# Kernel optimization log

Hardware: AMD Instinct MI355X
Metric: run time of the kernel (lower is better)

## Reference

```python
import jax, jax.numpy as jnp
import numpy as np

MAX_DISTANCE = 5
DISTANCE_TAU = 2.0
H, W = 4096, 4096


def _shifts_at_distance(distance):
    # All (dx, dy) with |dx| + |dy| == distance (diamond ring)
    return [(dx, dy)
            for dx in range(-distance, distance + 1)
            for dy in range(-distance, distance + 1)
            if abs(dx) + abs(dy) == distance]


def setup_inputs() -> dict:
    key = jax.random.key(0)
    grid_spikes = jax.random.normal(key, (H, W), dtype=jnp.float32)
    # Parameter init: w_d = exp(-d / tau), d = 1..max_distance
    distances = jnp.arange(1, MAX_DISTANCE + 1, dtype=jnp.float32)
    distance_weights = jnp.exp(-distances / DISTANCE_TAU)
    return {"grid_spikes": grid_spikes, "distance_weights": distance_weights}


def reference(grid_spikes, distance_weights):
    # I_internal = sum_{d=1}^{D} w_d * sum_{|dx|+|dy|=d} roll(s, (dx, dy))
    contributions = []
    for distance in range(1, MAX_DISTANCE + 1):
        ring = jnp.zeros_like(grid_spikes)
        for dx, dy in _shifts_at_distance(distance):
            ring = ring + jnp.roll(grid_spikes, shift=(dx, dy), axis=(0, 1))
        contributions.append(ring)
    all_neighbors = jnp.stack(contributions, axis=0)          # [D, H, W]
    total_input = (all_neighbors * distance_weights[:, None, None]).sum(axis=0)
    return total_input
```

## Files before the change

kernel.cpp:

```cpp
#include <hip/hip_runtime.h>
#include <stdint.h>


#define GMASK  4095
#define TR     8
#define NRW    (TR + 10)
#define SW     512
#define LW     (SW + 16)

typedef float f4 __attribute__((ext_vector_type(4), aligned(16)));

#define GLOBAL_AS __attribute__((address_space(1)))
#define LDS_AS    __attribute__((address_space(3)))

__device__ __forceinline__ void stage16(const float* g, float* l) {
    __builtin_amdgcn_global_load_lds((const GLOBAL_AS uint32_t*)g,
                                     (LDS_AS uint32_t*)l, 16, 0, 0);
}

__device__ __forceinline__ float uniform_f(float x) {
    union { float f; int i; } u;
    u.f = x;
    u.i = __builtin_amdgcn_readfirstlane(u.i);
    return u.f;
}

__global__ __launch_bounds__(128)
void diamond_stencil(const float* __restrict__ s, const float* __restrict__ w,
                     float* __restrict__ out)
{
    __shared__ float tile[NRW][LW];

    const int tid  = threadIdx.x;
    const int lane = tid & 63;
    const int wv   = tid >> 6;

    const int bid = blockIdx.x;
    const int xcd = bid & 7;
    const int i   = bid >> 3;
    const int bx  = i & 7;
    const int ys  = i >> 3;

    const int j0 = bx << 9;
    const int t0 = xcd * 512 + ys * TR;

#pragma unroll
    for (int m = 0; m < 9; ++m) {
        const int r = wv + 2 * m;
        const float* srow = s + ((size_t)((t0 - 5 + r) & GMASK) << 12);
        float* lrow = &tile[r][8];
        stage16(srow + j0 + lane * 4,       lrow);
        stage16(srow + j0 + 256 + lane * 4, lrow + 256);
    }

    if (tid < NRW * 4) {
        const int r  = tid >> 2, p = tid & 3;
        const int gc = (p < 2 ? j0 - 8 + p * 4 : j0 + SW + (p - 2) * 4) & GMASK;
        const int lc = (p < 2 ? p * 4 : 8 + SW + (p - 2) * 4);
        const float* srow = s + ((size_t)((t0 - 5 + r) & GMASK) << 12);
        *(f4*)&tile[r][lc] = *(const f4*)(srow + gc);
    }

    __syncthreads();

    float wgt[6];
    wgt[0] = 1.0f;
#pragma unroll
    for (int d = 1; d <= 5; ++d) wgt[d] = uniform_f(w[d - 1]);

    float acc[TR][4];
#pragma unroll
    for (int a = 0; a < TR; ++a)
#pragma unroll
        for (int c = 0; c < 4; ++c) acc[a][c] = 0.0f;

    const int tc = tid * 4;

#pragma unroll
    for (int r = 0; r < NRW; ++r) {
        const f4* lp = (const f4*)&tile[r][tc];
        const f4 A = lp[0], B = lp[1], C = lp[2], D = lp[3], E = lp[4];
        float f[20];
        f[0]=A.x; f[1]=A.y; f[2]=A.z; f[3]=A.w;
        f[4]=B.x; f[5]=B.y; f[6]=B.z; f[7]=B.w;
        f[8]=C.x; f[9]=C.y; f[10]=C.z; f[11]=C.w;
        f[12]=D.x; f[13]=D.y; f[14]=D.z; f[15]=D.w;
        f[16]=E.x; f[17]=E.y; f[18]=E.z; f[19]=E.w;

#pragma unroll
        for (int c = 0; c < 4; ++c) {
            const float ctr = f[8 + c];
            float Hs[6];
            Hs[0] = ctr;
#pragma unroll
            for (int k = 1; k <= 5; ++k)
                Hs[k] = Hs[k - 1] + wgt[k] * (f[8 + c - k] + f[8 + c + k]);

#pragma unroll
            for (int a = 0; a < TR; ++a) {
                const int d = r - 5 - a;
                if (d < -5 || d > 5) continue;
                if (d == 0)
                    acc[a][c] += Hs[5] - ctr;
                else {
                    const int ad = d < 0 ? -d : d;
                    acc[a][c] += wgt[ad] * Hs[5 - ad];
                }
            }
        }
    }

#pragma unroll
    for (int a = 0; a < TR; ++a) {
        float* op = out + ((size_t)(t0 + a) << 12) + j0 + tc;
        f4 r0;
        r0.x = acc[a][0]; r0.y = acc[a][1]; r0.z = acc[a][2]; r0.w = acc[a][3];
        __builtin_nontemporal_store(r0, (f4*)op);
    }
}

extern "C" void kernel_launch(void* const* d_in, const int* in_sizes, int n_in,
                              void* d_out, int out_size, void* d_ws, size_t ws_size,
                              hipStream_t stream)
{
    const float* s = (const float*)d_in[0];
    const float* w = (const float*)d_in[1];
    float* out = (float*)d_out;

    dim3 grid(4096);
    dim3 block(128);
    diamond_stencil<<<grid, block, 0, stream>>>(s, w, out);
}
```

Measured before the change: 121.6 us.

## Stream row bands through an LDS ring buffer with persistent blocks

Each block now walks down a 64-row band in eight 8-row tiles and keeps input rows in a 32-row LDS ring. The next tile's rows are loaded asynchronously while the current tile computes, so the 10-row halo is fetched once per band instead of once per tile. The grid shrinks from 4096 blocks to 512, and the output stores switch from nontemporal to plain stores. In exchange there are fewer blocks to fill the GPU, more serial work per block, and a barrier after every tile.

```diff
diff --git a/kernel.cpp b/kernel.cpp
--- a/kernel.cpp
+++ b/kernel.cpp
@@ -4,7 +4,8 @@
 
 #define GMASK  4095
 #define TR     8
-#define NRW    (TR + 10)
+#define NTILE  8
+#define RING   32
 #define SW     512
 #define LW     (SW + 16)
 
@@ -29,93 +30,103 @@
 void diamond_stencil(const float* __restrict__ s, const float* __restrict__ w,
                      float* __restrict__ out)
 {
-    __shared__ float tile[NRW][LW];
+    __shared__ float ring[RING][LW];
 
     const int tid  = threadIdx.x;
     const int lane = tid & 63;
     const int wv   = tid >> 6;
 
-    const int bid = blockIdx.x;
-    const int xcd = bid & 7;
-    const int i   = bid >> 3;
-    const int bx  = i & 7;
-    const int ys  = i >> 3;
+    const int bid   = blockIdx.x;
+    const int xcd   = bid & 7;
+    const int idx   = bid >> 3;
+    const int strip = idx & 7;
+    const int band  = xcd * 8 + (idx >> 3);
 
-    const int j0 = bx << 9;
-    const int t0 = xcd * 512 + ys * TR;
-
-#pragma unroll
-    for (int m = 0; m < 9; ++m) {
-        const int r = wv + 2 * m;
-        const float* srow = s + ((size_t)((t0 - 5 + r) & GMASK) << 12);
-        float* lrow = &tile[r][8];
-        stage16(srow + j0 + lane * 4,       lrow);
-        stage16(srow + j0 + 256 + lane * 4, lrow + 256);
-    }
-
-    if (tid < NRW * 4) {
-        const int r  = tid >> 2, p = tid & 3;
-        const int gc = (p < 2 ? j0 - 8 + p * 4 : j0 + SW + (p - 2) * 4) & GMASK;
-        const int lc = (p < 2 ? p * 4 : 8 + SW + (p - 2) * 4);
-        const float* srow = s + ((size_t)((t0 - 5 + r) & GMASK) << 12);
-        *(f4*)&tile[r][lc] = *(const f4*)(srow + gc);
-    }
-
-    __syncthreads();
+    const int j0  = strip << 9;
+    const int rb  = band << 6;
+    const int rb5 = rb - 5;
 
     float wgt[6];
     wgt[0] = 1.0f;
 #pragma unroll
     for (int d = 1; d <= 5; ++d) wgt[d] = uniform_f(w[d - 1]);
 
-    float acc[TR][4];
-#pragma unroll
-    for (int a = 0; a < TR; ++a)
-#pragma unroll
-        for (int c = 0; c < 4; ++c) acc[a][c] = 0.0f;
-
     const int tc = tid * 4;
 
+    auto stage_rows = [&](int n0, int cnt) {
+        for (int n = n0 + wv; n < n0 + cnt; n += 2) {
+            const float* srow = s + ((size_t)((rb5 + n) & GMASK) << 12);
+            float* lrow = &ring[n & (RING - 1)][8];
+            stage16(srow + j0 + lane * 4,       lrow);
+            stage16(srow + j0 + 256 + lane * 4, lrow + 256);
+        }
+        if (tid < cnt * 4) {
+            const int rr = tid >> 2, p = tid & 3;
+            const int n  = n0 + rr;
+            const int gc = (p < 2 ? j0 - 8 + p * 4 : j0 + SW + (p - 2) * 4) & GMASK;
+            const int lc = (p < 2 ? p * 4 : 8 + SW + (p - 2) * 4);
+            const float* srow = s + ((size_t)((rb5 + n) & GMASK) << 12);
+            *(f4*)&ring[n & (RING - 1)][lc] = *(const f4*)(srow + gc);
+        }
+    };
+
+    stage_rows(0, 18);
+    __syncthreads();
+
+    for (int t = 0; t < NTILE; ++t) {
+        if (t < NTILE - 1) stage_rows(18 + 8 * t, 8);
+
+        float acc[TR][4];
 #pragma unroll
-    for (int r = 0; r < NRW; ++r) {
-        const f4* lp = (const f4*)&tile[r][tc];
-        const f4 A = lp[0], B = lp[1], C = lp[2], D = lp[3], E = lp[4];
-        float f[20];
-        f[0]=A.x; f[1]=A.y; f[2]=A.z; f[3]=A.w;
-        f[4]=B.x; f[5]=B.y; f[6]=B.z; f[7]=B.w;
-        f[8]=C.x; f[9]=C.y; f[10]=C.z; f[11]=C.w;
-        f[12]=D.x; f[13]=D.y; f[14]=D.z; f[15]=D.w;
-        f[16]=E.x; f[17]=E.y; f[18]=E.z; f[19]=E.w;
+        for (int a = 0; a < TR; ++a)
+#pragma unroll
+            for (int c = 0; c < 4; ++c) acc[a][c] = 0.0f;
+
+        const int n0 = 8 * t;
+#pragma unroll
+        for (int k = 0; k < TR + 10; ++k) {
+            const int slot = (n0 + k) & (RING - 1);
+            const f4* lp = (const f4*)&ring[slot][tc];
+            const f4 A = lp[0], B = lp[1], C = lp[2], D = lp[3], E = lp[4];
+            float f[20];
+            f[0]=A.x;  f[1]=A.y;  f[2]=A.z;  f[3]=A.w;
+            f[4]=B.x;  f[5]=B.y;  f[6]=B.z;  f[7]=B.w;
+            f[8]=C.x;  f[9]=C.y;  f[10]=C.z; f[11]=C.w;
+            f[12]=D.x; f[13]=D.y; f[14]=D.z; f[15]=D.w;
+            f[16]=E.x; f[17]=E.y; f[18]=E.z; f[19]=E.w;
 
 #pragma unroll
-        for (int c = 0; c < 4; ++c) {
-            const float ctr = f[8 + c];
-            float Hs[6];
-            Hs[0] = ctr;
+            for (int c = 0; c < 4; ++c) {
+                const float ctr = f[8 + c];
+                float Hs[6];
+                Hs[0] = ctr;
 #pragma unroll
-            for (int k = 1; k <= 5; ++k)
-                Hs[k] = Hs[k - 1] + wgt[k] * (f[8 + c - k] + f[8 + c + k]);
+                for (int q = 1; q <= 5; ++q)
+                    Hs[q] = Hs[q - 1] + wgt[q] * (f[8 + c - q] + f[8 + c + q]);
 
 #pragma unroll
-            for (int a = 0; a < TR; ++a) {
-                const int d = r - 5 - a;
-                if (d < -5 || d > 5) continue;
-                if (d == 0)
-                    acc[a][c] += Hs[5] - ctr;
-                else {
-                    const int ad = d < 0 ? -d : d;
-                    acc[a][c] += wgt[ad] * Hs[5 - ad];
+                for (int a = 0; a < TR; ++a) {
+                    const int d = k - 5 - a;
+                    if (d < -5 || d > 5) continue;
+                    if (d == 0)
+                        acc[a][c] += Hs[5] - ctr;
+                    else {
+                        const int ad = d < 0 ? -d : d;
+                        acc[a][c] += wgt[ad] * Hs[5 - ad];
+                    }
                 }
             }
         }
-    }
 
 #pragma unroll
-    for (int a = 0; a < TR; ++a) {
-        float* op = out + ((size_t)(t0 + a) << 12) + j0 + tc;
-        f4 r0;
-        r0.x = acc[a][0]; r0.y = acc[a][1]; r0.z = acc[a][2]; r0.w = acc[a][3];
-        __builtin_nontemporal_store(r0, (f4*)op);
+        for (int a = 0; a < TR; ++a) {
+            float* op = out + ((size_t)(rb + 8 * t + a) << 12) + j0 + tc;
+            f4 r0;
+            r0.x = acc[a][0]; r0.y = acc[a][1]; r0.z = acc[a][2]; r0.w = acc[a][3];
+            *(f4*)op = r0;
+        }
+
+        __syncthreads();
     }
 }
 
@@ -127,7 +138,7 @@
     const float* w = (const float*)d_in[1];
     float* out = (float*)d_out;
 
-    dim3 grid(4096);
+    dim3 grid(512);
     dim3 block(128);
     diamond_stencil<<<grid, block, 0, stream>>>(s, w, out);
 }
```

Measured after the change: 125.3 us. 1.03x slower.
